# Kernel tuning notes

Measured on AMD Instinct MI355X. Metric: run time of the kernel, lower is better.

Reference implementation:

```python
import jax, jax.numpy as jnp
import numpy as np

NM = 16  # n_modes


def setup_inputs() -> dict:
    key = jax.random.key(0)
    k1, k2, k3, k4 = jax.random.split(key, 4)
    B, M, N, I, O = 8, 256, 256, 64, 64
    std = 1.0 / (I * O)
    x = jax.random.normal(k1, (B, M, N, I), dtype=jnp.float32)
    w1 = jax.random.normal(k2, (I, O, NM, NM, 2), dtype=jnp.float32) * std
    w2 = jax.random.normal(k3, (I, O, NM, NM, 2), dtype=jnp.float32) * std
    lin_w = jax.random.normal(k4, (O, O), dtype=jnp.float32) * (1.0 / np.sqrt(O))
    lin_b = jnp.zeros((O,), dtype=jnp.float32)
    return {"x": x, "w1": w1, "w2": w2, "lin_w": lin_w, "lin_b": lin_b}


def _to_complex(w):
    return jax.lax.complex(w[..., 0], w[..., 1])


def reference(x, w1, w2, lin_w, lin_b):
    B, M, N, I = x.shape
    O = w1.shape[1]
    # [B, I, M, N]
    xt = jnp.transpose(x, (0, 3, 1, 2))
    # rfft over last two dims -> [B, I, M, N//2 + 1] complex
    x_ft = jnp.fft.rfft2(xt, s=(M, N), axes=(-2, -1))
    w1c = _to_complex(w1)  # [I, O, NM, NM]
    w2c = _to_complex(w2)
    # truncated complex matmuls over low modes (top rows) and high-negative modes (bottom rows)
    out_top = jnp.einsum('bixy,ioxy->boxy', x_ft[:, :, :NM, :NM], w1c)
    out_bot = jnp.einsum('bixy,ioxy->boxy', x_ft[:, :, -NM:, :NM], w2c)
    zeros_mid = jnp.zeros((B, O, M - 2 * NM, NM), dtype=out_top.dtype)
    rows = jnp.concatenate([out_top, zeros_mid, out_bot], axis=2)  # [B, O, M, NM]
    zeros_right = jnp.zeros((B, O, M, N // 2 + 1 - NM), dtype=out_top.dtype)
    out_ft = jnp.concatenate([rows, zeros_right], axis=3)  # [B, O, M, N//2+1]
    y = jnp.fft.irfft2(out_ft, s=(M, N), axes=(-2, -1))  # real [B, O, M, N]
    y = jnp.transpose(y, (0, 2, 3, 1))  # [B, M, N, O]
    res = y @ lin_w + lin_b
    return jax.nn.relu(y + res)
```

## Files before the change

kernel.cpp:

```cpp
#include <hip/hip_runtime.h>
#include <hip/hip_bf16.h>
#include <math.h>


#define TOFF  65536
#define XOFF  (TOFF + 4194304)
#define YOFF  (XOFF + 524288)
#define GOFF  (YOFF + 524288)

__global__ __launch_bounds__(256) void setup_tables(const float* __restrict__ lin_w,
                                                    float* __restrict__ ws) {
    int j = blockIdx.x * 256 + threadIdx.x;
    const float ANG = 0.024543692606170259f;
    if (j < 4096) {
        int n = j >> 4, ky = j & 15;
        int a = (n * ky) & 255;
        float s, c; sincosf(ANG * (float)a, &s, &c);
        float* p = ws + n * 32 + ky * 2;
        p[0] = c; p[1] = -s;
    } else if (j < 12288) {
        int e = j - 4096; int m = e >> 5, kx = e & 31;
        int kxe = kx + (kx < 16 ? 0 : 224);
        int a = (m * kxe) & 255;
        float s, c; sincosf(ANG * (float)a, &s, &c);
        int g = kx >> 2, kl = kx & 3;
        float* p = ws + 8192 + g * 2048 + m * 8 + kl * 2;
        p[0] = c; p[1] = -s;
    } else if (j < 20480) {
        int e = j - 12288; int kx = e >> 8, m = e & 255;
        int kxe = kx + (kx < 16 ? 0 : 224);
        int a = (kxe * m) & 255;
        float s, c; sincosf(ANG * (float)a, &s, &c);
        float* p = ws + 24576 + (kx * 256 + m) * 2;
        p[0] = c * (1.0f / 256.0f);
        p[1] = s * (1.0f / 256.0f);
    } else if (j < 28672) {
        int e = j - 20480; int f = e >> 8, n = e & 255;
        int ky = f >> 1, h = f & 1;
        int a = (ky * n) & 255;
        float s, c; sincosf(ANG * (float)a, &s, &c);
        float scale = (ky == 0 ? 1.0f : 2.0f) * (1.0f / 256.0f);
        ws[40960 + f * 256 + n] = h ? (-scale * s) : (scale * c);
    } else if (j < 32768) {
        int e = j - 28672;
        int op = e >> 6, o = e & 63;
        ws[49152 + e] = lin_w[e] + ((op == o) ? 1.0f : 0.0f);
    }
}

__global__ __launch_bounds__(256) void stageA(const float* __restrict__ x,
                                              const float* __restrict__ tabA,
                                              float* __restrict__ T) {
    __shared__ float red[2 * 8 * 64 * 2];
    int bid = blockIdx.x;
    int b = bid >> 8, m = bid & 255;
    int t = threadIdx.x;
    int i = t & 63, w = t >> 6;
    int kh = w & 1, h = w >> 1;
    const float* xp = x + (size_t)bid * 16384 + (size_t)h * 8192 + i;
    const float* twp = tabA + __builtin_amdgcn_readfirstlane(h * 4096 + kh * 16);
    float aR[8], aI[8];
#pragma unroll
    for (int j = 0; j < 8; ++j) { aR[j] = 0.f; aI[j] = 0.f; }
#pragma unroll 4
    for (int nn = 0; nn < 128; ++nn) {
        float xv = xp[nn * 64];
        const float* tp = twp + nn * 32;
#pragma unroll
        for (int j = 0; j < 8; ++j) {
            aR[j] = fmaf(tp[2 * j], xv, aR[j]);
            aI[j] = fmaf(tp[2 * j + 1], xv, aI[j]);
        }
    }
    float2* rp = (float2*)red + (kh * 8) * 64 + i;
    if (h == 1) {
#pragma unroll
        for (int j = 0; j < 8; ++j) rp[j * 64] = make_float2(aR[j], aI[j]);
    }
    __syncthreads();
    if (h == 0) {
        float2* Tb = (float2*)T;
#pragma unroll
        for (int j = 0; j < 8; ++j) {
            float2 p = rp[j * 64];
            int ky = kh * 8 + j;
            Tb[((size_t)(b * 16 + ky) * 256 + m) * 64 + i] =
                make_float2(aR[j] + p.x, aI[j] + p.y);
        }
    }
}

__global__ __launch_bounds__(512) void stageB(const float* __restrict__ T,
                                              const float* __restrict__ twF,
                                              float* __restrict__ X) {
    __shared__ float red[4 * 4 * 64 * 2];
    int bid = blockIdx.x;
    int b = bid >> 5;
    int ky = (bid >> 1) & 15;
    int half = bid & 1;
    int t = threadIdx.x, i = t & 63;
    int q = (t >> 6) & 3, h = t >> 8;
    int Q = half * 4 + q;
    const float2* Tp = (const float2*)T + (size_t)(b * 16 + ky) * 256 * 64 + i;
    const float* tw = twF + __builtin_amdgcn_readfirstlane(Q * 2048);
    float r0 = 0, r1 = 0, r2 = 0, r3 = 0;
    float s0 = 0, s1 = 0, s2 = 0, s3 = 0;
    int m0 = h * 128;
#pragma unroll 4
    for (int mm = 0; mm < 128; ++mm) {
        int m = m0 + mm;
        float2 tv = Tp[(size_t)m * 64];
        const float* tp = tw + m * 8;
        r0 = fmaf(tv.x, tp[0], fmaf(-tv.y, tp[1], r0));
        s0 = fmaf(tv.x, tp[1], fmaf( tv.y, tp[0], s0));
        r1 = fmaf(tv.x, tp[2], fmaf(-tv.y, tp[3], r1));
        s1 = fmaf(tv.x, tp[3], fmaf( tv.y, tp[2], s1));
        r2 = fmaf(tv.x, tp[4], fmaf(-tv.y, tp[5], r2));
        s2 = fmaf(tv.x, tp[5], fmaf( tv.y, tp[4], s2));
        r3 = fmaf(tv.x, tp[6], fmaf(-tv.y, tp[7], r3));
        s3 = fmaf(tv.x, tp[7], fmaf( tv.y, tp[6], s3));
    }
    float2* rp = (float2*)red + (q * 4) * 64 + i;
    if (h == 1) {
        rp[0 * 64] = make_float2(r0, s0);
        rp[1 * 64] = make_float2(r1, s1);
        rp[2 * 64] = make_float2(r2, s2);
        rp[3 * 64] = make_float2(r3, s3);
    }
    __syncthreads();
    if (h == 0) {
        float2 p0 = rp[0 * 64], p1 = rp[1 * 64], p2 = rp[2 * 64], p3 = rp[3 * 64];
        r0 += p0.x; s0 += p0.y; r1 += p1.x; s1 += p1.y;
        r2 += p2.x; s2 += p2.y; r3 += p3.x; s3 += p3.y;
        int kx0 = Q * 4;
        float2* Xb = (float2*)X;
        size_t base = ((size_t)(b * 16 + ky) * 32 + kx0) * 64 + i;
        Xb[base + 0 * 64] = make_float2(r0, s0);
        Xb[base + 1 * 64] = make_float2(r1, s1);
        Xb[base + 2 * 64] = make_float2(r2, s2);
        Xb[base + 3 * 64] = make_float2(r3, s3);
    }
}

__global__ __launch_bounds__(256) void stageC(const float* __restrict__ Xg,
                                              const float* __restrict__ w1,
                                              const float* __restrict__ w2,
                                              const float* __restrict__ Wf,
                                              float* __restrict__ Y2) {
    __shared__ float Ws[64 * 64 * 2];
    __shared__ float Xs[8 * 64 * 2];
    __shared__ float Ys[8 * 64 * 2];
    __shared__ float Wfs[64 * 64];
    int bid = blockIdx.x;
    int kx = bid & 31, ky = bid >> 5;
    int t = threadIdx.x;
    const float* wsrc = (kx < 16) ? w1 : w2;
    int xx = kx & 15;
#pragma unroll
    for (int q = 0; q < 16; ++q) {
        int p = t + q * 256;
        int ii = p >> 6, oo = p & 63;
        float2 wv = *(const float2*)(wsrc + ((size_t)(ii * 64 + oo) * 256 + xx * 16 + ky) * 2);
        ((float2*)Ws)[ii * 64 + oo] = wv;
    }
#pragma unroll
    for (int q = 0; q < 2; ++q) {
        int p = t + q * 256;
        int bb = p >> 6, ii = p & 63;
        ((float2*)Xs)[bb * 64 + ii] =
            ((const float2*)Xg)[((size_t)(bb * 16 + ky) * 32 + kx) * 64 + ii];
    }
#pragma unroll
    for (int q = 0; q < 16; ++q) Wfs[t + q * 256] = Wf[t + q * 256];
    __syncthreads();
    int o = t & 63, bg = t >> 6;
    float yr0 = 0, yi0 = 0, yr1 = 0, yi1 = 0;
    for (int ii = 0; ii < 64; ++ii) {
        float2 w = ((float2*)Ws)[ii * 64 + o];
        float2 xa = ((float2*)Xs)[bg * 64 + ii];
        float2 xb = ((float2*)Xs)[(bg + 4) * 64 + ii];
        yr0 = fmaf(xa.x, w.x, fmaf(-xa.y, w.y, yr0));
        yi0 = fmaf(xa.x, w.y, fmaf( xa.y, w.x, yi0));
        yr1 = fmaf(xb.x, w.x, fmaf(-xb.y, w.y, yr1));
        yi1 = fmaf(xb.x, w.y, fmaf( xb.y, w.x, yi1));
    }
    ((float2*)Ys)[bg * 64 + o] = make_float2(yr0, yi0);
    ((float2*)Ys)[(bg + 4) * 64 + o] = make_float2(yr1, yi1);
    __syncthreads();
    float zr0 = 0, zi0 = 0, zr1 = 0, zi1 = 0;
    for (int op = 0; op < 64; ++op) {
        float wf = Wfs[op * 64 + o];
        float2 ya = ((float2*)Ys)[bg * 64 + op];
        float2 yb = ((float2*)Ys)[(bg + 4) * 64 + op];
        zr0 = fmaf(ya.x, wf, zr0); zi0 = fmaf(ya.y, wf, zi0);
        zr1 = fmaf(yb.x, wf, zr1); zi1 = fmaf(yb.y, wf, zi1);
    }
    float2* Yb = (float2*)Y2;
    Yb[((size_t)(bg * 32 + kx) * 16 + ky) * 64 + o] = make_float2(zr0, zi0);
    Yb[((size_t)((bg + 4) * 32 + kx) * 16 + ky) * 64 + o] = make_float2(zr1, zi1);
}

__global__ __launch_bounds__(512) void stageD(const float* __restrict__ Y2,
                                              const float* __restrict__ twI,
                                              float* __restrict__ G) {
    __shared__ float Ysl[16 * 64 * 2];
    int bid = blockIdx.x;
    int b = bid >> 5, mg = bid & 31;
    int t = threadIdx.x, o = t & 63, ml = t >> 6;
    int m = mg * 8 + ml;
    float gr[16], gi[16];
#pragma unroll
    for (int k = 0; k < 16; ++k) { gr[k] = 0.f; gi[k] = 0.f; }
    for (int kx = 0; kx < 32; ++kx) {
        __syncthreads();
        const float2* src = (const float2*)Y2 + (size_t)(b * 32 + kx) * 1024;
#pragma unroll
        for (int qq = 0; qq < 2; ++qq) ((float2*)Ysl)[t + qq * 512] = src[t + qq * 512];
        __syncthreads();
        int off = __builtin_amdgcn_readfirstlane((kx * 256 + m) * 2);
        float c = twI[off], d = twI[off + 1];
#pragma unroll
        for (int ky = 0; ky < 16; ++ky) {
            float2 yv = ((float2*)Ysl)[ky * 64 + o];
            gr[ky] = fmaf(yv.x, c, fmaf(-yv.y, d, gr[ky]));
            gi[ky] = fmaf(yv.x, d, fmaf( yv.y, c, gi[ky]));
        }
    }
    float2* Gb = (float2*)G;
#pragma unroll
    for (int ky = 0; ky < 16; ++ky)
        Gb[((size_t)(b * 256 + m) * 16 + ky) * 64 + o] = make_float2(gr[ky], gi[ky]);
}

__global__ __launch_bounds__(256) void stageE(const float* __restrict__ G,
                                              const float* __restrict__ tabE,
                                              const float* __restrict__ lin_b,
                                              float* __restrict__ out) {
    __shared__ float Bs[32 * 256];
    __shared__ float Hs[32 * 64];
    int bid = blockIdx.x;
    int t = threadIdx.x;
    const float4* tE4 = (const float4*)tabE;
#pragma unroll
    for (int q = 0; q < 8; ++q) ((float4*)Bs)[t + q * 256] = tE4[t + q * 256];
    const float2* Gp = (const float2*)G + (size_t)bid * 1024;
#pragma unroll
    for (int q = 0; q < 4; ++q) {
        int p = t + q * 256;
        int ky = p >> 6, o = p & 63;
        float2 g = Gp[p];
        Hs[(2 * ky) * 64 + o] = g.x;
        Hs[(2 * ky + 1) * 64 + o] = g.y;
    }
    __syncthreads();
    int o4 = (t & 15) * 4, n0 = (t >> 4) * 16;
    float acc[16][4];
#pragma unroll
    for (int j = 0; j < 16; ++j) { acc[j][0] = acc[j][1] = acc[j][2] = acc[j][3] = 0.f; }
    for (int f = 0; f < 32; ++f) {
        float4 h = *(const float4*)(Hs + f * 64 + o4);
        const float* bp = Bs + f * 256 + n0;
        float4 a0 = *(const float4*)(bp);
        float4 a1 = *(const float4*)(bp + 4);
        float4 a2 = *(const float4*)(bp + 8);
        float4 a3 = *(const float4*)(bp + 12);
        float av[16] = {a0.x, a0.y, a0.z, a0.w, a1.x, a1.y, a1.z, a1.w,
                        a2.x, a2.y, a2.z, a2.w, a3.x, a3.y, a3.z, a3.w};
#pragma unroll
        for (int j = 0; j < 16; ++j) {
            acc[j][0] = fmaf(av[j], h.x, acc[j][0]);
            acc[j][1] = fmaf(av[j], h.y, acc[j][1]);
            acc[j][2] = fmaf(av[j], h.z, acc[j][2]);
            acc[j][3] = fmaf(av[j], h.w, acc[j][3]);
        }
    }
    float4 bias = *(const float4*)(lin_b + o4);
    float* outp = out + (size_t)bid * 256 * 64;
#pragma unroll
    for (int j = 0; j < 16; ++j) {
        int n = n0 + j;
        float4 r;
        r.x = fmaxf(acc[j][0] + bias.x, 0.f);
        r.y = fmaxf(acc[j][1] + bias.y, 0.f);
        r.z = fmaxf(acc[j][2] + bias.z, 0.f);
        r.w = fmaxf(acc[j][3] + bias.w, 0.f);
        *(float4*)(outp + (size_t)n * 64 + o4) = r;
    }
}

extern "C" void kernel_launch(void* const* d_in, const int* in_sizes, int n_in,
                              void* d_out, int out_size, void* d_ws, size_t ws_size,
                              hipStream_t stream) {
    const float* x     = (const float*)d_in[0];
    const float* w1    = (const float*)d_in[1];
    const float* w2    = (const float*)d_in[2];
    const float* lin_w = (const float*)d_in[3];
    const float* lin_b = (const float*)d_in[4];
    float* ws  = (float*)d_ws;
    float* out = (float*)d_out;

    float* T  = ws + TOFF;
    float* X  = ws + XOFF;
    float* Y2 = ws + YOFF;
    float* G  = ws + GOFF;

    setup_tables<<<128, 256, 0, stream>>>(lin_w, ws);
    stageA<<<2048, 256, 0, stream>>>(x, ws, T);
    stageB<<<256, 512, 0, stream>>>(T, ws + 8192, X);
    stageC<<<512, 256, 0, stream>>>(X, w1, w2, ws + 49152, Y2);
    stageD<<<256, 512, 0, stream>>>(Y2, ws + 24576, G);
    stageE<<<2048, 256, 0, stream>>>(G, ws + 40960, lin_b, out);
}
```

Baseline: 162.3 us.

## Restructure stageA to process two rows per wave with register double-buffered loads

stageA now has each wave compute two full m-rows over all 256 n, so every twiddle load is reused across two rows. The old split of n into halves, with its shared-memory reduction and barrier, is gone. x loads are software-pipelined through two register buffers so the next group loads while the FMAs run. The grid shrinks from 2048 to 512 blocks, which lowers parallelism and raises register pressure per thread.

```diff
diff --git a/kernel.cpp b/kernel.cpp
--- a/kernel.cpp
+++ b/kernel.cpp
@@ -51,43 +51,80 @@
 __global__ __launch_bounds__(256) void stageA(const float* __restrict__ x,
                                               const float* __restrict__ tabA,
                                               float* __restrict__ T) {
-    __shared__ float red[2 * 8 * 64 * 2];
-    int bid = blockIdx.x;
-    int b = bid >> 8, m = bid & 255;
+    int bid = blockIdx.x;
+    int b = bid >> 6, mq = bid & 63;
     int t = threadIdx.x;
     int i = t & 63, w = t >> 6;
-    int kh = w & 1, h = w >> 1;
-    const float* xp = x + (size_t)bid * 16384 + (size_t)h * 8192 + i;
-    const float* twp = tabA + __builtin_amdgcn_readfirstlane(h * 4096 + kh * 16);
-    float aR[8], aI[8];
-#pragma unroll
-    for (int j = 0; j < 8; ++j) { aR[j] = 0.f; aI[j] = 0.f; }
-#pragma unroll 4
-    for (int nn = 0; nn < 128; ++nn) {
-        float xv = xp[nn * 64];
-        const float* tp = twp + nn * 32;
-#pragma unroll
-        for (int j = 0; j < 8; ++j) {
-            aR[j] = fmaf(tp[2 * j], xv, aR[j]);
-            aI[j] = fmaf(tp[2 * j + 1], xv, aI[j]);
-        }
-    }
-    float2* rp = (float2*)red + (kh * 8) * 64 + i;
-    if (h == 1) {
-#pragma unroll
-        for (int j = 0; j < 8; ++j) rp[j * 64] = make_float2(aR[j], aI[j]);
-    }
-    __syncthreads();
-    if (h == 0) {
-        float2* Tb = (float2*)T;
-#pragma unroll
-        for (int j = 0; j < 8; ++j) {
-            float2 p = rp[j * 64];
-            int ky = kh * 8 + j;
-            Tb[((size_t)(b * 16 + ky) * 256 + m) * 64 + i] =
-                make_float2(aR[j] + p.x, aI[j] + p.y);
-        }
-    }
+    int kh = w & 1, mp = w >> 1;
+    int m_a = mq * 4 + mp * 2;
+    const float* xpa = x + (size_t)(b * 256 + m_a) * 16384 + i;
+    const float* xpb = xpa + 16384;
+    const float* twp = tabA + __builtin_amdgcn_readfirstlane(kh * 16);
+    float aR[2][8], aI[2][8];
+#pragma unroll
+    for (int j = 0; j < 2; ++j)
+#pragma unroll
+        for (int k = 0; k < 8; ++k) { aR[j][k] = 0.f; aI[j][k] = 0.f; }
+
+    float A0[8], A1[8];
+#pragma unroll
+    for (int q = 0; q < 4; ++q) { A0[q] = xpa[q * 64]; A0[4 + q] = xpb[q * 64]; }
+
+    for (int g = 0; g < 64; g += 2) {
+        int n0 = g * 4;
+        {
+            const float* pa = xpa + (size_t)(n0 + 4) * 64;
+            const float* pb = xpb + (size_t)(n0 + 4) * 64;
+#pragma unroll
+            for (int q = 0; q < 4; ++q) { A1[q] = pa[q * 64]; A1[4 + q] = pb[q * 64]; }
+        }
+        {
+            const float* tp = twp + (size_t)n0 * 32;
+#pragma unroll
+            for (int q = 0; q < 4; ++q) {
+                const float* tq = tp + q * 32;
+#pragma unroll
+                for (int k = 0; k < 8; ++k) {
+                    float c = tq[2 * k], s = tq[2 * k + 1];
+                    aR[0][k] = fmaf(c, A0[q], aR[0][k]);
+                    aI[0][k] = fmaf(s, A0[q], aI[0][k]);
+                    aR[1][k] = fmaf(c, A0[4 + q], aR[1][k]);
+                    aI[1][k] = fmaf(s, A0[4 + q], aI[1][k]);
+                }
+            }
+        }
+        {
+            int n2 = (g + 2 < 64) ? (n0 + 8) : 0;
+            const float* pa = xpa + (size_t)n2 * 64;
+            const float* pb = xpb + (size_t)n2 * 64;
+#pragma unroll
+            for (int q = 0; q < 4; ++q) { A0[q] = pa[q * 64]; A0[4 + q] = pb[q * 64]; }
+        }
+        {
+            const float* tp = twp + (size_t)(n0 + 4) * 32;
+#pragma unroll
+            for (int q = 0; q < 4; ++q) {
+                const float* tq = tp + q * 32;
+#pragma unroll
+                for (int k = 0; k < 8; ++k) {
+                    float c = tq[2 * k], s = tq[2 * k + 1];
+                    aR[0][k] = fmaf(c, A1[q], aR[0][k]);
+                    aI[0][k] = fmaf(s, A1[q], aI[0][k]);
+                    aR[1][k] = fmaf(c, A1[4 + q], aR[1][k]);
+                    aI[1][k] = fmaf(s, A1[4 + q], aI[1][k]);
+                }
+            }
+        }
+    }
+    float2* Tb = (float2*)T;
+#pragma unroll
+    for (int j = 0; j < 2; ++j)
+#pragma unroll
+        for (int k = 0; k < 8; ++k) {
+            int ky = kh * 8 + k;
+            Tb[((size_t)(b * 16 + ky) * 256 + (m_a + j)) * 64 + i] =
+                make_float2(aR[j][k], aI[j][k]);
+        }
 }
 
 __global__ __launch_bounds__(512) void stageB(const float* __restrict__ T,
@@ -305,7 +342,7 @@
     float* G  = ws + GOFF;
 
     setup_tables<<<128, 256, 0, stream>>>(lin_w, ws);
-    stageA<<<2048, 256, 0, stream>>>(x, ws, T);
+    stageA<<<512, 256, 0, stream>>>(x, ws, T);
     stageB<<<256, 512, 0, stream>>>(T, ws + 8192, X);
     stageC<<<512, 256, 0, stream>>>(X, w1, w2, ws + 49152, Y2);
     stageD<<<256, 512, 0, stream>>>(Y2, ws + 24576, G);
```

Measured after the change: 167.6 us. 1.03x slower.

## Register-tile stageA DFT with float4 loads and shuffle reduction; widen stageB tiles

Applied to the files above, without the earlier changes.

StageA now has each thread load float4 chunks of x and twiddles and accumulate a 4x4 register tile of (channel, ky) outputs. Partial sums are reduced across the n-split with warp shuffles instead of a shared-memory reduction and barrier. StageB is retiled so each wave computes 8 kx outputs from float4 twiddle loads, which halves the grid to 128 blocks, and the twiddle table layout changes to match. The aim is more arithmetic per load and fewer barriers, at the cost of lower stageB occupancy (fewer blocks) and extra select logic in stageA.

```diff
diff --git a/kernel.cpp b/kernel.cpp
--- a/kernel.cpp
+++ b/kernel.cpp
@@ -23,8 +23,8 @@
         int kxe = kx + (kx < 16 ? 0 : 224);
         int a = (m * kxe) & 255;
         float s, c; sincosf(ANG * (float)a, &s, &c);
-        int g = kx >> 2, kl = kx & 3;
-        float* p = ws + 8192 + g * 2048 + m * 8 + kl * 2;
+        int oc = kx >> 3, kl = kx & 7;
+        float* p = ws + 8192 + oc * 4096 + m * 16 + kl * 2;
         p[0] = c; p[1] = -s;
     } else if (j < 20480) {
         int e = j - 12288; int kx = e >> 8, m = e & 255;
@@ -51,94 +51,108 @@
 __global__ __launch_bounds__(256) void stageA(const float* __restrict__ x,
                                               const float* __restrict__ tabA,
                                               float* __restrict__ T) {
-    __shared__ float red[2 * 8 * 64 * 2];
     int bid = blockIdx.x;
     int b = bid >> 8, m = bid & 255;
     int t = threadIdx.x;
-    int i = t & 63, w = t >> 6;
-    int kh = w & 1, h = w >> 1;
-    const float* xp = x + (size_t)bid * 16384 + (size_t)h * 8192 + i;
-    const float* twp = tabA + __builtin_amdgcn_readfirstlane(h * 4096 + kh * 16);
-    float aR[8], aI[8];
-#pragma unroll
-    for (int j = 0; j < 8; ++j) { aR[j] = 0.f; aI[j] = 0.f; }
+    int kq = t >> 6;
+    int l = t & 63;
+    int su = l >> 4, j = l & 15;
+    const float* xp  = x + (size_t)bid * 16384 + su * 64 + j * 4;
+    const float* twp = tabA + su * 32 + kq * 8;
+    float accR[4][4], accI[4][4];
+#pragma unroll
+    for (int ii = 0; ii < 4; ++ii)
+#pragma unroll
+        for (int k = 0; k < 4; ++k) { accR[ii][k] = 0.f; accI[ii][k] = 0.f; }
+
 #pragma unroll 4
-    for (int nn = 0; nn < 128; ++nn) {
-        float xv = xp[nn * 64];
-        const float* tp = twp + nn * 32;
-#pragma unroll
-        for (int j = 0; j < 8; ++j) {
-            aR[j] = fmaf(tp[2 * j], xv, aR[j]);
-            aI[j] = fmaf(tp[2 * j + 1], xv, aI[j]);
+    for (int n0 = 0; n0 < 256; n0 += 4) {
+        float4 xv = *(const float4*)(xp + (size_t)n0 * 64);
+        float4 t0 = *(const float4*)(twp + (size_t)n0 * 32);
+        float4 t1 = *(const float4*)(twp + (size_t)n0 * 32 + 4);
+#define CPLX(K, C, S)                                                       \
+        accR[0][K] = fmaf(C, xv.x, accR[0][K]); accI[0][K] = fmaf(S, xv.x, accI[0][K]); \
+        accR[1][K] = fmaf(C, xv.y, accR[1][K]); accI[1][K] = fmaf(S, xv.y, accI[1][K]); \
+        accR[2][K] = fmaf(C, xv.z, accR[2][K]); accI[2][K] = fmaf(S, xv.z, accI[2][K]); \
+        accR[3][K] = fmaf(C, xv.w, accR[3][K]); accI[3][K] = fmaf(S, xv.w, accI[3][K]);
+        CPLX(0, t0.x, t0.y)
+        CPLX(1, t0.z, t0.w)
+        CPLX(2, t1.x, t1.y)
+        CPLX(3, t1.z, t1.w)
+#undef CPLX
+    }
+#pragma unroll
+    for (int ii = 0; ii < 4; ++ii)
+#pragma unroll
+        for (int k = 0; k < 4; ++k) {
+            float r = accR[ii][k];
+            r += __shfl_xor(r, 16); r += __shfl_xor(r, 32);
+            accR[ii][k] = r;
+            float q = accI[ii][k];
+            q += __shfl_xor(q, 16); q += __shfl_xor(q, 32);
+            accI[ii][k] = q;
         }
-    }
-    float2* rp = (float2*)red + (kh * 8) * 64 + i;
-    if (h == 1) {
-#pragma unroll
-        for (int j = 0; j < 8; ++j) rp[j * 64] = make_float2(aR[j], aI[j]);
-    }
-    __syncthreads();
-    if (h == 0) {
-        float2* Tb = (float2*)T;
-#pragma unroll
-        for (int j = 0; j < 8; ++j) {
-            float2 p = rp[j * 64];
-            int ky = kh * 8 + j;
-            Tb[((size_t)(b * 16 + ky) * 256 + m) * 64 + i] =
-                make_float2(aR[j] + p.x, aI[j] + p.y);
-        }
-    }
+    float selR[4], selI[4];
+#pragma unroll
+    for (int ii = 0; ii < 4; ++ii) {
+        selR[ii] = su == 0 ? accR[ii][0] : su == 1 ? accR[ii][1]
+                 : su == 2 ? accR[ii][2] : accR[ii][3];
+        selI[ii] = su == 0 ? accI[ii][0] : su == 1 ? accI[ii][1]
+                 : su == 2 ? accI[ii][2] : accI[ii][3];
+    }
+    int ky = kq * 4 + su;
+    float* Tf = T + (((size_t)(b * 16 + ky) * 256 + m) * 64 + 4 * j) * 2;
+    *(float4*)Tf       = make_float4(selR[0], selI[0], selR[1], selI[1]);
+    *(float4*)(Tf + 4) = make_float4(selR[2], selI[2], selR[3], selI[3]);
 }
 
 __global__ __launch_bounds__(512) void stageB(const float* __restrict__ T,
                                               const float* __restrict__ twF,
                                               float* __restrict__ X) {
-    __shared__ float red[4 * 4 * 64 * 2];
-    int bid = blockIdx.x;
-    int b = bid >> 5;
-    int ky = (bid >> 1) & 15;
-    int half = bid & 1;
+    __shared__ float red[4 * 8 * 64 * 2];
+    int bid = blockIdx.x;
+    int b = bid >> 4;
+    int ky = bid & 15;
     int t = threadIdx.x, i = t & 63;
-    int q = (t >> 6) & 3, h = t >> 8;
-    int Q = half * 4 + q;
-    const float2* Tp = (const float2*)T + (size_t)(b * 16 + ky) * 256 * 64 + i;
-    const float* tw = twF + __builtin_amdgcn_readfirstlane(Q * 2048);
-    float r0 = 0, r1 = 0, r2 = 0, r3 = 0;
-    float s0 = 0, s1 = 0, s2 = 0, s3 = 0;
-    int m0 = h * 128;
+    int w = t >> 6, oc = w & 3, smh = w >> 2;
+    int m0 = smh * 128;
+    const float2* Tp = (const float2*)T + (size_t)(b * 16 + ky) * 16384 + i;
+    const float* twp = twF + oc * 4096;
+    float aR[8], aI[8];
+#pragma unroll
+    for (int k = 0; k < 8; ++k) { aR[k] = 0.f; aI[k] = 0.f; }
 #pragma unroll 4
     for (int mm = 0; mm < 128; ++mm) {
         int m = m0 + mm;
         float2 tv = Tp[(size_t)m * 64];
-        const float* tp = tw + m * 8;
-        r0 = fmaf(tv.x, tp[0], fmaf(-tv.y, tp[1], r0));
-        s0 = fmaf(tv.x, tp[1], fmaf( tv.y, tp[0], s0));
-        r1 = fmaf(tv.x, tp[2], fmaf(-tv.y, tp[3], r1));
-        s1 = fmaf(tv.x, tp[3], fmaf( tv.y, tp[2], s1));
-        r2 = fmaf(tv.x, tp[4], fmaf(-tv.y, tp[5], r2));
-        s2 = fmaf(tv.x, tp[5], fmaf( tv.y, tp[4], s2));
-        r3 = fmaf(tv.x, tp[6], fmaf(-tv.y, tp[7], r3));
-        s3 = fmaf(tv.x, tp[7], fmaf( tv.y, tp[6], s3));
-    }
-    float2* rp = (float2*)red + (q * 4) * 64 + i;
-    if (h == 1) {
-        rp[0 * 64] = make_float2(r0, s0);
-        rp[1 * 64] = make_float2(r1, s1);
-        rp[2 * 64] = make_float2(r2, s2);
-        rp[3 * 64] = make_float2(r3, s3);
+        const float* tp = twp + m * 16;
+        float4 w0 = *(const float4*)(tp);
+        float4 w1 = *(const float4*)(tp + 4);
+        float4 w2 = *(const float4*)(tp + 8);
+        float4 w3 = *(const float4*)(tp + 12);
+#define CMUL(K, C, S)                                             \
+        aR[K] = fmaf(tv.x, C, fmaf(-tv.y, S, aR[K]));             \
+        aI[K] = fmaf(tv.x, S, fmaf( tv.y, C, aI[K]));
+        CMUL(0, w0.x, w0.y) CMUL(1, w0.z, w0.w)
+        CMUL(2, w1.x, w1.y) CMUL(3, w1.z, w1.w)
+        CMUL(4, w2.x, w2.y) CMUL(5, w2.z, w2.w)
+        CMUL(6, w3.x, w3.y) CMUL(7, w3.z, w3.w)
+#undef CMUL
+    }
+    float2* rp = (float2*)red + (oc * 8) * 64 + i;
+    if (smh == 1) {
+#pragma unroll
+        for (int k = 0; k < 8; ++k) rp[k * 64] = make_float2(aR[k], aI[k]);
     }
     __syncthreads();
-    if (h == 0) {
-        float2 p0 = rp[0 * 64], p1 = rp[1 * 64], p2 = rp[2 * 64], p3 = rp[3 * 64];
-        r0 += p0.x; s0 += p0.y; r1 += p1.x; s1 += p1.y;
-        r2 += p2.x; s2 += p2.y; r3 += p3.x; s3 += p3.y;
-        int kx0 = Q * 4;
+    if (smh == 0) {
         float2* Xb = (float2*)X;
-        size_t base = ((size_t)(b * 16 + ky) * 32 + kx0) * 64 + i;
-        Xb[base + 0 * 64] = make_float2(r0, s0);
-        Xb[base + 1 * 64] = make_float2(r1, s1);
-        Xb[base + 2 * 64] = make_float2(r2, s2);
-        Xb[base + 3 * 64] = make_float2(r3, s3);
+        size_t base = ((size_t)(b * 16 + ky) * 32 + oc * 8) * 64 + i;
+#pragma unroll
+        for (int k = 0; k < 8; ++k) {
+            float2 p = rp[k * 64];
+            Xb[base + (size_t)k * 64] = make_float2(aR[k] + p.x, aI[k] + p.y);
+        }
     }
 }
 
@@ -217,8 +231,8 @@
 #pragma unroll
         for (int qq = 0; qq < 2; ++qq) ((float2*)Ysl)[t + qq * 512] = src[t + qq * 512];
         __syncthreads();
-        int off = __builtin_amdgcn_readfirstlane((kx * 256 + m) * 2);
-        float c = twI[off], d = twI[off + 1];
+        float2 cd = *(const float2*)(twI + (size_t)(kx * 256 + m) * 2);
+        float c = cd.x, d = cd.y;
 #pragma unroll
         for (int ky = 0; ky < 16; ++ky) {
             float2 yv = ((float2*)Ysl)[ky * 64 + o];
@@ -306,7 +320,7 @@
 
     setup_tables<<<128, 256, 0, stream>>>(lin_w, ws);
     stageA<<<2048, 256, 0, stream>>>(x, ws, T);
-    stageB<<<256, 512, 0, stream>>>(T, ws + 8192, X);
+    stageB<<<128, 512, 0, stream>>>(T, ws + 8192, X);
     stageC<<<512, 256, 0, stream>>>(X, w1, w2, ws + 49152, Y2);
     stageD<<<256, 512, 0, stream>>>(Y2, ws + 24576, G);
     stageE<<<2048, 256, 0, stream>>>(G, ws + 40960, lin_b, out);
```

Measured after the change: 198.7 us. 22.4% more time.

## Restructure stageA to process two rows per block with LDS twiddle table

Applied to the files above, without the earlier changes.

StageA now handles two m-rows per block, with each of the four waves covering a quarter of n and computing all 16 ky outputs. Twiddles are staged once into shared memory and read as float4, so each twiddle value is reused across both rows. Partials are combined by a two-level shared-memory tree reduction before writing T. This cuts global twiddle traffic and halves the grid, at the cost of more accumulator registers (64 floats) and extra barriers. StageD's twiddle load also changes from a readfirstlane scalar load to a per-thread float2 load.

```diff
diff --git a/kernel.cpp b/kernel.cpp
--- a/kernel.cpp
+++ b/kernel.cpp
@@ -51,42 +51,90 @@
 __global__ __launch_bounds__(256) void stageA(const float* __restrict__ x,
                                               const float* __restrict__ tabA,
                                               float* __restrict__ T) {
-    __shared__ float red[2 * 8 * 64 * 2];
-    int bid = blockIdx.x;
-    int b = bid >> 8, m = bid & 255;
+    __shared__ float sm[8192];
+    int bid = blockIdx.x;
+    int b = bid >> 7, mp = bid & 127;
+    int m0 = mp * 2;
     int t = threadIdx.x;
     int i = t & 63, w = t >> 6;
-    int kh = w & 1, h = w >> 1;
-    const float* xp = x + (size_t)bid * 16384 + (size_t)h * 8192 + i;
-    const float* twp = tabA + __builtin_amdgcn_readfirstlane(h * 4096 + kh * 16);
-    float aR[8], aI[8];
-#pragma unroll
-    for (int j = 0; j < 8; ++j) { aR[j] = 0.f; aI[j] = 0.f; }
-#pragma unroll 4
-    for (int nn = 0; nn < 128; ++nn) {
-        float xv = xp[nn * 64];
-        const float* tp = twp + nn * 32;
-#pragma unroll
-        for (int j = 0; j < 8; ++j) {
-            aR[j] = fmaf(tp[2 * j], xv, aR[j]);
-            aI[j] = fmaf(tp[2 * j + 1], xv, aI[j]);
+    {
+        const float4* src = (const float4*)tabA;
+        float4* dst = (float4*)sm;
+#pragma unroll
+        for (int q = 0; q < 8; ++q) dst[t + q * 256] = src[t + q * 256];
+    }
+    __syncthreads();
+
+    const float* xp0 = x + (((size_t)(b * 256 + m0) * 256) + w * 64) * 64 + i;
+    const float* xp1 = xp0 + 16384;
+    float aR[2][16], aI[2][16];
+#pragma unroll
+    for (int mm = 0; mm < 2; ++mm)
+#pragma unroll
+        for (int k = 0; k < 16; ++k) { aR[mm][k] = 0.f; aI[mm][k] = 0.f; }
+
+    const float* twb = sm + w * 64 * 32;
+#pragma unroll 2
+    for (int nn = 0; nn < 64; ++nn) {
+        float x0 = xp0[(size_t)nn * 64];
+        float x1 = xp1[(size_t)nn * 64];
+        const float* tp = twb + nn * 32;
+#pragma unroll
+        for (int q = 0; q < 8; ++q) {
+            float4 tv = *(const float4*)(tp + q * 4);
+            int k0 = 2 * q, k1 = 2 * q + 1;
+            aR[0][k0] = fmaf(tv.x, x0, aR[0][k0]); aI[0][k0] = fmaf(tv.y, x0, aI[0][k0]);
+            aR[1][k0] = fmaf(tv.x, x1, aR[1][k0]); aI[1][k0] = fmaf(tv.y, x1, aI[1][k0]);
+            aR[0][k1] = fmaf(tv.z, x0, aR[0][k1]); aI[0][k1] = fmaf(tv.w, x0, aI[0][k1]);
+            aR[1][k1] = fmaf(tv.z, x1, aR[1][k1]); aI[1][k1] = fmaf(tv.w, x1, aI[1][k1]);
         }
     }
-    float2* rp = (float2*)red + (kh * 8) * 64 + i;
-    if (h == 1) {
-#pragma unroll
-        for (int j = 0; j < 8; ++j) rp[j * 64] = make_float2(aR[j], aI[j]);
-    }
-    __syncthreads();
-    if (h == 0) {
+
+    __syncthreads();
+    if (w == 1 || w == 3) {
+        float* rp = sm + ((w == 1) ? 0 : 4096) + i;
+#pragma unroll
+        for (int mm = 0; mm < 2; ++mm)
+#pragma unroll
+            for (int k = 0; k < 16; ++k) {
+                rp[(mm * 32 + 2 * k) * 64]     = aR[mm][k];
+                rp[(mm * 32 + 2 * k + 1) * 64] = aI[mm][k];
+            }
+    }
+    __syncthreads();
+    if (w == 0 || w == 2) {
+        const float* rp = sm + ((w == 0) ? 0 : 4096) + i;
+#pragma unroll
+        for (int mm = 0; mm < 2; ++mm)
+#pragma unroll
+            for (int k = 0; k < 16; ++k) {
+                aR[mm][k] += rp[(mm * 32 + 2 * k) * 64];
+                aI[mm][k] += rp[(mm * 32 + 2 * k + 1) * 64];
+            }
+    }
+    __syncthreads();
+    if (w == 2) {
+        float* rp = sm + i;
+#pragma unroll
+        for (int mm = 0; mm < 2; ++mm)
+#pragma unroll
+            for (int k = 0; k < 16; ++k) {
+                rp[(mm * 32 + 2 * k) * 64]     = aR[mm][k];
+                rp[(mm * 32 + 2 * k + 1) * 64] = aI[mm][k];
+            }
+    }
+    __syncthreads();
+    if (w == 0) {
+        const float* rp = sm + i;
         float2* Tb = (float2*)T;
 #pragma unroll
-        for (int j = 0; j < 8; ++j) {
-            float2 p = rp[j * 64];
-            int ky = kh * 8 + j;
-            Tb[((size_t)(b * 16 + ky) * 256 + m) * 64 + i] =
-                make_float2(aR[j] + p.x, aI[j] + p.y);
-        }
+        for (int mm = 0; mm < 2; ++mm)
+#pragma unroll
+            for (int k = 0; k < 16; ++k) {
+                float r = aR[mm][k] + rp[(mm * 32 + 2 * k) * 64];
+                float q = aI[mm][k] + rp[(mm * 32 + 2 * k + 1) * 64];
+                Tb[((size_t)(b * 16 + k) * 256 + (m0 + mm)) * 64 + i] = make_float2(r, q);
+            }
     }
 }
 
@@ -217,8 +265,8 @@
 #pragma unroll
         for (int qq = 0; qq < 2; ++qq) ((float2*)Ysl)[t + qq * 512] = src[t + qq * 512];
         __syncthreads();
-        int off = __builtin_amdgcn_readfirstlane((kx * 256 + m) * 2);
-        float c = twI[off], d = twI[off + 1];
+        float2 cd = *(const float2*)(twI + (size_t)(kx * 256 + m) * 2);
+        float c = cd.x, d = cd.y;
 #pragma unroll
         for (int ky = 0; ky < 16; ++ky) {
             float2 yv = ((float2*)Ysl)[ky * 64 + o];
@@ -305,7 +353,7 @@
     float* G  = ws + GOFF;
 
     setup_tables<<<128, 256, 0, stream>>>(lin_w, ws);
-    stageA<<<2048, 256, 0, stream>>>(x, ws, T);
+    stageA<<<1024, 256, 0, stream>>>(x, ws, T);
     stageB<<<256, 512, 0, stream>>>(T, ws + 8192, X);
     stageC<<<512, 256, 0, stream>>>(X, w1, w2, ws + 49152, Y2);
     stageD<<<256, 512, 0, stream>>>(Y2, ws + 24576, G);
```

Result: faster. 156.8 us (-3.4%).
